# Performance work log

Hardware: AMD Instinct MI355X
Metric: run time of the kernel (lower is better)

## Reference

```python
import jax, jax.numpy as jnp
import numpy as np

N, E = 4096, 131072
IN_DIM, HID, OUT_DIM = 128, 64, 128
H1 = 4                       # gat1 heads
D_MODEL = HID * H1           # 256
NHEAD = 4
D_FF = 2048


def setup_inputs() -> dict:
    key = jax.random.key(0)
    ks = jax.random.split(key, 16)
    def w(k, shape, scale=0.05):
        return jax.random.normal(k, shape, dtype=jnp.float32) * scale
    return {
        "x": jax.random.normal(ks[0], (N, IN_DIM), dtype=jnp.float32),
        "edge_index": jax.random.randint(ks[1], (2, E), 0, N, dtype=jnp.int32),
        "gat1_w": w(ks[2], (H1 * HID, IN_DIM)),
        "gat1_asrc": w(ks[3], (H1, HID)),
        "gat1_adst": w(ks[4], (H1, HID)),
        "gat1_b": jnp.zeros((H1 * HID,), jnp.float32),
        "in_proj_w": w(ks[5], (3 * D_MODEL, D_MODEL)),
        "in_proj_b": jnp.zeros((3 * D_MODEL,), jnp.float32),
        "out_proj_w": w(ks[6], (D_MODEL, D_MODEL)),
        "out_proj_b": jnp.zeros((D_MODEL,), jnp.float32),
        "lin1_w": w(ks[7], (D_FF, D_MODEL)),
        "lin1_b": jnp.zeros((D_FF,), jnp.float32),
        "lin2_w": w(ks[8], (D_MODEL, D_FF)),
        "lin2_b": jnp.zeros((D_MODEL,), jnp.float32),
        "ln1_g": jnp.ones((D_MODEL,), jnp.float32),
        "ln1_b": jnp.zeros((D_MODEL,), jnp.float32),
        "ln2_g": jnp.ones((D_MODEL,), jnp.float32),
        "ln2_b": jnp.zeros((D_MODEL,), jnp.float32),
        "gat2_w": w(ks[9], (OUT_DIM, D_MODEL)),
        "gat2_asrc": w(ks[10], (1, OUT_DIM)),
        "gat2_adst": w(ks[11], (1, OUT_DIM)),
        "gat2_b": jnp.zeros((OUT_DIM,), jnp.float32),
    }


def _add_self_loops(ei, n):
    loops = jnp.arange(n, dtype=ei.dtype)
    return jnp.concatenate([ei, jnp.stack([loops, loops])], axis=1)


def _segment_softmax(logits, seg, n):
    # numerically stable softmax over edges grouped by destination node
    m = jax.ops.segment_max(logits, seg, num_segments=n)
    m = jnp.where(jnp.isfinite(m), m, 0.0)
    e = jnp.exp(logits - m[seg])
    s = jax.ops.segment_sum(e, seg, num_segments=n)
    return e / (s[seg] + 1e-16)


def _gat(x, ei, W, asrc, adst, b, heads, out_ch):
    n = x.shape[0]
    h = (x @ W.T).reshape(n, heads, out_ch)          # [N,H,C]
    al_s = jnp.einsum('nhc,hc->nh', h, asrc)
    al_d = jnp.einsum('nhc,hc->nh', h, adst)
    src, dst = ei[0], ei[1]
    logits = jax.nn.leaky_relu(al_s[src] + al_d[dst], 0.2)   # [E,H]
    alpha = _segment_softmax(logits, dst, n)
    out = jax.ops.segment_sum(h[src] * alpha[:, :, None], dst, num_segments=n)
    return out.reshape(n, heads * out_ch) + b


def _ln(x, g, b):
    mu = x.mean(-1, keepdims=True)
    v = x.var(-1, keepdims=True)
    return (x - mu) / jnp.sqrt(v + 1e-5) * g + b


def _forward(x, edge_index, gat1_w, gat1_asrc, gat1_adst, gat1_b,
             in_proj_w, in_proj_b, out_proj_w, out_proj_b,
             lin1_w, lin1_b, lin2_w, lin2_b, ln1_g, ln1_b, ln2_g, ln2_b,
             gat2_w, gat2_asrc, gat2_adst, gat2_b):
    n = x.shape[0]
    ei = _add_self_loops(edge_index, n)
    h = jax.nn.elu(_gat(x, ei, gat1_w, gat1_asrc, gat1_adst, gat1_b, H1, HID))  # [N, 256]
    # TransformerEncoderLayer (post-norm, relu, no dropout in eval)
    hd = D_MODEL // NHEAD
    qkv = h @ in_proj_w.T + in_proj_b
    q, k, v = jnp.split(qkv, 3, axis=-1)
    q = q.reshape(n, NHEAD, hd)
    k = k.reshape(n, NHEAD, hd)
    v = v.reshape(n, NHEAD, hd)
    scores = jnp.einsum('qhd,khd->hqk', q, k) / jnp.sqrt(jnp.float32(hd))
    attn = jax.nn.softmax(scores, axis=-1)
    o = jnp.einsum('hqk,khd->qhd', attn, v).reshape(n, D_MODEL)
    o = o @ out_proj_w.T + out_proj_b
    h = _ln(h + o, ln1_g, ln1_b)
    ff = jax.nn.relu(h @ lin1_w.T + lin1_b) @ lin2_w.T + lin2_b
    h = _ln(h + ff, ln2_g, ln2_b)
    return _gat(h, ei, gat2_w, gat2_asrc, gat2_adst, gat2_b, 1, OUT_DIM)


def reference(x, edge_index, gat1_w, gat1_asrc, gat1_adst, gat1_b,
              in_proj_w, in_proj_b, out_proj_w, out_proj_b,
              lin1_w, lin1_b, lin2_w, lin2_b, ln1_g, ln1_b, ln2_g, ln2_b,
              gat2_w, gat2_asrc, gat2_adst, gat2_b):
    return _forward(x, edge_index, gat1_w, gat1_asrc, gat1_adst, gat1_b,
                    in_proj_w, in_proj_b, out_proj_w, out_proj_b,
                    lin1_w, lin1_b, lin2_w, lin2_b, ln1_g, ln1_b, ln2_g, ln2_b,
                    gat2_w, gat2_asrc, gat2_adst, gat2_b)
```

## Files before the change

### kernel.cpp

```cpp
#include <hip/hip_runtime.h>
#include <hip/hip_bf16.h>
#include <math.h>

#define NN 4096
#define NE 131072
#define EE (NE + NN)

typedef unsigned short u16;
typedef short s8v __attribute__((ext_vector_type(8)));
typedef float f4v __attribute__((ext_vector_type(4)));
typedef float f16v __attribute__((ext_vector_type(16)));

__device__ inline u16 f2b(float f) {
  __hip_bfloat16 h = __float2bfloat16(f);
  return __builtin_bit_cast(u16, h);
}
__device__ inline float b2f(u16 v) {
  unsigned int u = ((unsigned int)v) << 16;
  return __builtin_bit_cast(float, u);
}

__global__ void k_count(const int* __restrict__ ei, int* __restrict__ deg) {
  int e = blockIdx.x * 256 + threadIdx.x;
  if (e >= EE) return;
  int dst = (e < NE) ? ei[NE + e] : (e - NE);
  atomicAdd(&deg[dst], 1);
}

__global__ __launch_bounds__(1024) void k_scan(const int* __restrict__ deg, int* __restrict__ rowptr) {
  __shared__ int lds[1024];
  int t = threadIdx.x;
  int v0 = deg[t*4+0], v1 = deg[t*4+1], v2 = deg[t*4+2], v3 = deg[t*4+3];
  int s1 = v0+v1, s2 = s1+v2, s3 = s2+v3;
  lds[t] = s3;
  __syncthreads();
  for (int off = 1; off < 1024; off <<= 1) {
    int add = (t >= off) ? lds[t-off] : 0;
    __syncthreads();
    lds[t] += add;
    __syncthreads();
  }
  int base = lds[t] - s3;
  rowptr[t*4+1] = base + v0;
  rowptr[t*4+2] = base + s1;
  rowptr[t*4+3] = base + s2;
  rowptr[t*4+4] = base + s3;
  if (t == 0) rowptr[0] = 0;
}

__global__ void k_scatter(const int* __restrict__ ei, const int* __restrict__ rowptr,
                          int* __restrict__ cursor, int* __restrict__ csr_src) {
  int e = blockIdx.x * 256 + threadIdx.x;
  if (e >= EE) return;
  int src, dst;
  if (e < NE) { src = ei[e]; dst = ei[NE + e]; }
  else { src = e - NE; dst = src; }
  int pos = rowptr[dst] + atomicAdd(&cursor[dst], 1);
  csr_src[pos] = src;
}

__global__ __launch_bounds__(256) void k_f2b_all(
    const float* a0, u16* b0, int e0, const float* a1, u16* b1, int e1,
    const float* a2, u16* b2, int e2, const float* a3, u16* b3, int e3,
    const float* a4, u16* b4, int e4, const float* a5, u16* b5, int e5,
    const float* a6, u16* b6, int e6)
{
  int i = blockIdx.x * 256 + threadIdx.x;
  const float* s; u16* d; int base;
  if      (i < e0) { s=a0; d=b0; base=0;  }
  else if (i < e1) { s=a1; d=b1; base=e0; }
  else if (i < e2) { s=a2; d=b2; base=e1; }
  else if (i < e3) { s=a3; d=b3; base=e2; }
  else if (i < e4) { s=a4; d=b4; base=e3; }
  else if (i < e5) { s=a5; d=b5; base=e4; }
  else if (i < e6) { s=a6; d=b6; base=e5; }
  else return;
  int j = i - base;
  float4 v = ((const float4*)s)[j];
  u16 r[4] = {f2b(v.x), f2b(v.y), f2b(v.z), f2b(v.w)};
  *(uint2*)(d + (size_t)j*4) = *(uint2*)r;
}

template<int HEADS, int C>
__global__ __launch_bounds__(256) void k_alogits(
    const u16* __restrict__ featb, const float* __restrict__ asrc,
    const float* __restrict__ adst, float* __restrict__ als, float* __restrict__ ald)
{
  constexpr int F = HEADS * C;
  int n = blockIdx.x, t = threadIdx.x;
  __shared__ float red[F];
  float f = b2f(featb[(size_t)n*F + t]);
  int hh = t / C, cc = t % C;
  red[t] = f * asrc[t];
  __syncthreads();
  for (int off = C/2; off > 0; off >>= 1) {
    float add = (cc < off) ? red[t + off] : 0.f;
    __syncthreads();
    if (cc < off) red[t] += add;
    __syncthreads();
  }
  if (cc == 0) als[(size_t)n*HEADS + hh] = red[t];
  __syncthreads();
  red[t] = f * adst[t];
  __syncthreads();
  for (int off = C/2; off > 0; off >>= 1) {
    float add = (cc < off) ? red[t + off] : 0.f;
    __syncthreads();
    if (cc < off) red[t] += add;
    __syncthreads();
  }
  if (cc == 0) ald[(size_t)n*HEADS + hh] = red[t];
}

template<int HEADS, int C, bool DO_ELU, bool WB>
__global__ __launch_bounds__(256) void k_gat_agg(
    const u16* __restrict__ featb, const float* __restrict__ als,
    const float* __restrict__ ald, const float* __restrict__ bias,
    const int* __restrict__ rowptr, const int* __restrict__ csr_src,
    float* __restrict__ out, u16* __restrict__ outb)
{
  constexpr int F = HEADS * C;
  int n = blockIdx.x, t = threadIdx.x;
  __shared__ float m_sh[HEADS], s_sh[HEADS];
  int start = rowptr[n];
  int deg = rowptr[n+1] - start;
  int lane = t & 63, wv = t >> 6;
  for (int hh = wv; hh < HEADS; hh += F/64) {
    float adl = ald[(size_t)n*HEADS + hh];
    float mx = -INFINITY;
    for (int i = lane; i < deg; i += 64) {
      int s = csr_src[start + i];
      float lg = als[(size_t)s*HEADS + hh] + adl;
      lg = (lg > 0.f) ? lg : 0.2f * lg;
      mx = fmaxf(mx, lg);
    }
    #pragma unroll
    for (int off = 32; off; off >>= 1) mx = fmaxf(mx, __shfl_xor(mx, off));
    float sm = 0.f;
    for (int i = lane; i < deg; i += 64) {
      int s = csr_src[start + i];
      float lg = als[(size_t)s*HEADS + hh] + adl;
      lg = (lg > 0.f) ? lg : 0.2f * lg;
      sm += expf(lg - mx);
    }
    #pragma unroll
    for (int off = 32; off; off >>= 1) sm += __shfl_xor(sm, off);
    if (lane == 0) { m_sh[hh] = mx; s_sh[hh] = sm; }
  }
  __syncthreads();
  int hh = t / C;
  float adl = ald[(size_t)n*HEADS + hh];
  float mh = m_sh[hh];
  float acc0 = 0.f, acc1 = 0.f;
  int i = 0;
  for (; i + 1 < deg; i += 2) {
    int s0 = csr_src[start + i];
    int s1 = csr_src[start + i + 1];
    float lg0 = als[(size_t)s0*HEADS + hh] + adl;
    float lg1 = als[(size_t)s1*HEADS + hh] + adl;
    lg0 = (lg0 > 0.f) ? lg0 : 0.2f * lg0;
    lg1 = (lg1 > 0.f) ? lg1 : 0.2f * lg1;
    float p0 = expf(lg0 - mh);
    float p1 = expf(lg1 - mh);
    acc0 += p0 * b2f(featb[(size_t)s0*F + t]);
    acc1 += p1 * b2f(featb[(size_t)s1*F + t]);
  }
  if (i < deg) {
    int s0 = csr_src[start + i];
    float lg0 = als[(size_t)s0*HEADS + hh] + adl;
    lg0 = (lg0 > 0.f) ? lg0 : 0.2f * lg0;
    acc0 += expf(lg0 - mh) * b2f(featb[(size_t)s0*F + t]);
  }
  float o = (acc0 + acc1) / (s_sh[hh] + 1e-16f) + bias[t];
  if (DO_ELU) o = (o > 0.f) ? o : (expf(o) - 1.f);
  out[(size_t)n*F + t] = o;
  if (WB) outb[(size_t)n*F + t] = f2b(o);
}

template<int MODE>
__global__ __launch_bounds__(256) void k_gemm_mfma(
    const u16* __restrict__ A, const u16* __restrict__ B,
    const float* __restrict__ bias, float* __restrict__ Cf, u16* __restrict__ Cb,
    u16* __restrict__ Qb, u16* __restrict__ Kb, u16* __restrict__ Vt,
    int M, int N, int K)
{
  __shared__ u16 Al[64*64];
  __shared__ u16 Bl[64*64];
  char* Ab = (char*)Al;
  char* Bb = (char*)Bl;
  const int t = threadIdx.x;
  const int lane = t & 63;
  const int lr = lane & 15, lk = lane >> 4;
  const int wid = t >> 6;
  const int wm = wid & 1, wn = wid >> 1;
  const int m0 = blockIdx.y * 64, n0 = blockIdx.x * 64;

  f4v acc[2][2];
  #pragma unroll
  for (int mi = 0; mi < 2; ++mi)
    #pragma unroll
    for (int ni = 0; ni < 2; ++ni)
      acc[mi][ni] = f4v{0.f, 0.f, 0.f, 0.f};

  for (int k0 = 0; k0 < K; k0 += 64) {
    #pragma unroll
    for (int i = 0; i < 2; ++i) {
      int idx = t + i*256;
      int row = idx >> 3, ch = idx & 7;
      s8v av = *(const s8v*)(A + (size_t)(m0 + row)*K + k0 + ch*8);
      *(s8v*)(Ab + row*128 + ((ch*16) ^ ((row & 7) << 4))) = av;
      s8v bv = *(const s8v*)(B + (size_t)(n0 + row)*K + k0 + ch*8);
      *(s8v*)(Bb + row*128 + ((ch*16) ^ ((row & 7) << 4))) = bv;
    }
    __syncthreads();
    #pragma unroll
    for (int ks = 0; ks < 2; ++ks) {
      s8v af[2], bfr[2];
      #pragma unroll
      for (int mi = 0; mi < 2; ++mi) {
        int row = wm*32 + mi*16 + lr;
        int ch = ks*4 + lk;
        af[mi] = *(const s8v*)(Ab + row*128 + ((ch*16) ^ ((row & 7) << 4)));
      }
      #pragma unroll
      for (int ni = 0; ni < 2; ++ni) {
        int row = wn*32 + ni*16 + lr;
        int ch = ks*4 + lk;
        bfr[ni] = *(const s8v*)(Bb + row*128 + ((ch*16) ^ ((row & 7) << 4)));
      }
      #pragma unroll
      for (int mi = 0; mi < 2; ++mi)
        #pragma unroll
        for (int ni = 0; ni < 2; ++ni)
          acc[mi][ni] = __builtin_amdgcn_mfma_f32_16x16x32_bf16(af[mi], bfr[ni], acc[mi][ni], 0, 0, 0);
    }
    __syncthreads();
  }
  #pragma unroll
  for (int ni = 0; ni < 2; ++ni) {
    int col = n0 + wn*32 + ni*16 + lr;
    float bc = bias ? bias[col] : 0.f;
    #pragma unroll
    for (int mi = 0; mi < 2; ++mi) {
      int row0 = m0 + wm*32 + mi*16 + lk*4;
      float v[4];
      #pragma unroll
      for (int r = 0; r < 4; ++r) {
        v[r] = acc[mi][ni][r] + bc;
        if (MODE == 1) v[r] = fmaxf(v[r], 0.f);
      }
      if (MODE == 0) {
        #pragma unroll
        for (int r = 0; r < 4; ++r) Cf[(size_t)(row0 + r)*N + col] = v[r];
      } else if (MODE == 1 || MODE == 2) {
        #pragma unroll
        for (int r = 0; r < 4; ++r) Cb[(size_t)(row0 + r)*N + col] = f2b(v[r]);
      } else {
        if (col < 512) {
          int head = (col >> 6) & 3;
          int d = col & 63;
          u16* dst = ((col < 256) ? Qb : Kb) + (size_t)head*262144 + d;
          #pragma unroll
          for (int r = 0; r < 4; ++r) dst[(size_t)(row0 + r)*64] = f2b(v[r]);
        } else {
          int cc = col - 512;
          int head = cc >> 6;
          int d = cc & 63;
          int quad = row0 & 12;
          int qs = (quad == 4) ? 8 : ((quad == 8) ? 4 : quad);
          size_t nphys = (size_t)((row0 & ~15) | qs);
          u16 o4[4];
          #pragma unroll
          for (int r = 0; r < 4; ++r) o4[r] = f2b(v[r]);
          *(uint2*)(Vt + (size_t)head*262144 + (size_t)d*4096 + nphys) = *(uint2*)o4;
        }
      }
    }
  }
}

__global__ __launch_bounds__(256) void k_gemm_sk(
    const u16* __restrict__ A, const u16* __restrict__ B,
    float* __restrict__ Po, int M, int N, int K)
{
  __shared__ u16 Al[64*64];
  __shared__ u16 Bl[64*64];
  char* Ab = (char*)Al;
  char* Bb = (char*)Bl;
  const int t = threadIdx.x;
  const int lane = t & 63;
  const int lr = lane & 15, lk = lane >> 4;
  const int wid = t >> 6;
  const int wm = wid & 1, wn = wid >> 1;
  const int m0 = blockIdx.y * 64, n0 = blockIdx.x * 64;
  const int z = blockIdx.z;
  const int ksl = K >> 2;

  f4v acc[2][2];
  #pragma unroll
  for (int mi = 0; mi < 2; ++mi)
    #pragma unroll
    for (int ni = 0; ni < 2; ++ni)
      acc[mi][ni] = f4v{0.f, 0.f, 0.f, 0.f};

  for (int k0 = z*ksl; k0 < (z+1)*ksl; k0 += 64) {
    #pragma unroll
    for (int i = 0; i < 2; ++i) {
      int idx = t + i*256;
      int row = idx >> 3, ch = idx & 7;
      s8v av = *(const s8v*)(A + (size_t)(m0 + row)*K + k0 + ch*8);
      *(s8v*)(Ab + row*128 + ((ch*16) ^ ((row & 7) << 4))) = av;
      s8v bv = *(const s8v*)(B + (size_t)(n0 + row)*K + k0 + ch*8);
      *(s8v*)(Bb + row*128 + ((ch*16) ^ ((row & 7) << 4))) = bv;
    }
    __syncthreads();
    #pragma unroll
    for (int ks = 0; ks < 2; ++ks) {
      s8v af[2], bfr[2];
      #pragma unroll
      for (int mi = 0; mi < 2; ++mi) {
        int row = wm*32 + mi*16 + lr;
        int ch = ks*4 + lk;
        af[mi] = *(const s8v*)(Ab + row*128 + ((ch*16) ^ ((row & 7) << 4)));
      }
      #pragma unroll
      for (int ni = 0; ni < 2; ++ni) {
        int row = wn*32 + ni*16 + lr;
        int ch = ks*4 + lk;
        bfr[ni] = *(const s8v*)(Bb + row*128 + ((ch*16) ^ ((row & 7) << 4)));
      }
      #pragma unroll
      for (int mi = 0; mi < 2; ++mi)
        #pragma unroll
        for (int ni = 0; ni < 2; ++ni)
          acc[mi][ni] = __builtin_amdgcn_mfma_f32_16x16x32_bf16(af[mi], bfr[ni], acc[mi][ni], 0, 0, 0);
    }
    __syncthreads();
  }
  float* Pz = Po + (size_t)z * M * N;
  #pragma unroll
  for (int ni = 0; ni < 2; ++ni) {
    int col = n0 + wn*32 + ni*16 + lr;
    #pragma unroll
    for (int mi = 0; mi < 2; ++mi) {
      int row0 = m0 + wm*32 + mi*16 + lk*4;
      #pragma unroll
      for (int r = 0; r < 4; ++r)
        Pz[(size_t)(row0 + r)*N + col] = acc[mi][ni][r];
    }
  }
}

template<bool WB>
__global__ __launch_bounds__(256) void k_ln(
    const float* __restrict__ a, const float* __restrict__ res,
    const float* __restrict__ g, const float* __restrict__ bb,
    float* __restrict__ out, u16* __restrict__ outb)
{
  int n = blockIdx.x, t = threadIdx.x;
  __shared__ float part[4];
  float v = a[(size_t)n*256 + t] + res[(size_t)n*256 + t];
  float s = v;
  #pragma unroll
  for (int off = 32; off; off >>= 1) s += __shfl_xor(s, off);
  if ((t & 63) == 0) part[t >> 6] = s;
  __syncthreads();
  float mean = (part[0] + part[1] + part[2] + part[3]) * (1.f/256.f);
  __syncthreads();
  float d = v - mean;
  float s2 = d * d;
  #pragma unroll
  for (int off = 32; off; off >>= 1) s2 += __shfl_xor(s2, off);
  if ((t & 63) == 0) part[t >> 6] = s2;
  __syncthreads();
  float var = (part[0] + part[1] + part[2] + part[3]) * (1.f/256.f);
  float rstd = rsqrtf(var + 1e-5f);
  float o = d * rstd * g[t] + bb[t];
  out[(size_t)n*256 + t] = o;
  if (WB) outb[(size_t)n*256 + t] = f2b(o);
}

template<bool WB>
__global__ __launch_bounds__(256) void k_ln_sk(
    const float* __restrict__ Po, const float* __restrict__ bias,
    const float* __restrict__ res, const float* __restrict__ g,
    const float* __restrict__ bb, float* __restrict__ out, u16* __restrict__ outb)
{
  int n = blockIdx.x, t = threadIdx.x;
  __shared__ float part[4];
  const size_t MN = (size_t)NN * 256;
  size_t idx = (size_t)n*256 + t;
  float v = Po[idx] + Po[MN + idx] + Po[2*MN + idx] + Po[3*MN + idx]
          + bias[t] + res[idx];
  float s = v;
  #pragma unroll
  for (int off = 32; off; off >>= 1) s += __shfl_xor(s, off);
  if ((t & 63) == 0) part[t >> 6] = s;
  __syncthreads();
  float mean = (part[0] + part[1] + part[2] + part[3]) * (1.f/256.f);
  __syncthreads();
  float d = v - mean;
  float s2 = d * d;
  #pragma unroll
  for (int off = 32; off; off >>= 1) s2 += __shfl_xor(s2, off);
  if ((t & 63) == 0) part[t >> 6] = s2;
  __syncthreads();
  float var = (part[0] + part[1] + part[2] + part[3]) * (1.f/256.f);
  float rstd = rsqrtf(var + 1e-5f);
  float o = d * rstd * g[t] + bb[t];
  out[idx] = o;
  if (WB) outb[idx] = f2b(o);
}

__global__ __launch_bounds__(512) void k_attn2(
    const u16* __restrict__ Qb, const u16* __restrict__ Kb,
    const u16* __restrict__ Vt, u16* __restrict__ attno_b)
{
  const int strip = blockIdx.x;
  const int head  = blockIdx.y;
  const int q0 = strip * 32;
  const int t = threadIdx.x;
  const int s = t >> 6;
  const int l = t & 63;
  const int lq = l & 31;
  const int lh = l >> 5;

  __shared__ float lds_O[4][32][68];
  __shared__ float lds_m[4][32];
  __shared__ float lds_l[4][32];

  const u16* Qh = Qb + (size_t)head * (4096*64);
  const u16* Kh = Kb + (size_t)head * (4096*64);
  const u16* Vh = Vt + (size_t)head * (64*4096);

  s8v qf[4];
#pragma unroll
  for (int dc = 0; dc < 4; ++dc)
    qf[dc] = *(const s8v*)(Qh + (size_t)(q0 + lq)*64 + dc*16 + lh*8);

  f16v accO[2];
#pragma unroll
  for (int dm = 0; dm < 2; ++dm)
#pragma unroll
    for (int i = 0; i < 16; ++i) accO[dm][i] = 0.f;

  float mrow = -INFINITY, lrow = 0.f;
  const float CE = 0.18033688011112042f;

  const int kt0 = s * 512;
  for (int kt = kt0; kt < kt0 + 512; kt += 64) {
    f16v st[2];
#pragma unroll
    for (int c = 0; c < 2; ++c)
#pragma unroll
      for (int i = 0; i < 16; ++i) st[c][i] = 0.f;
    __builtin_amdgcn_s_setprio(1);
#pragma unroll
    for (int dc = 0; dc < 4; ++dc) {
      s8v kf0 = *(const s8v*)(Kh + (size_t)(kt + lq)*64 + dc*16 + lh*8);
      s8v kf1 = *(const s8v*)(Kh + (size_t)(kt + 32 + lq)*64 + dc*16 + lh*8);
      st[0] = __builtin_amdgcn_mfma_f32_32x32x16_bf16(kf0, qf[dc], st[0], 0, 0, 0);
      st[1] = __builtin_amdgcn_mfma_f32_32x32x16_bf16(kf1, qf[dc], st[1], 0, 0, 0);
    }
    __builtin_amdgcn_s_setprio(0);
    float tm[16];
#pragma unroll
    for (int i = 0; i < 8; ++i) tm[i]   = fmaxf(st[0][2*i], st[0][2*i+1]);
#pragma unroll
    for (int i = 0; i < 8; ++i) tm[8+i] = fmaxf(st[1][2*i], st[1][2*i+1]);
#pragma unroll
    for (int w = 8; w >= 1; w >>= 1)
#pragma unroll
      for (int i = 0; i < 8; ++i) if (i < w) tm[i] = fmaxf(tm[i], tm[i+w]);
    float mx = fmaxf(tm[0], __shfl_xor(tm[0], 32));
    float mn;
    if (__all(mx - mrow <= 66.0f)) {
      mn = mrow;
    } else {
      mn = fmaxf(mrow, mx);
      float sc = exp2f((mrow - mn) * CE);
      mrow = mn;
      lrow *= sc;
#pragma unroll
      for (int dm = 0; dm < 2; ++dm)
#pragma unroll
        for (int i = 0; i < 16; ++i) accO[dm][i] *= sc;
    }
    float ts[16];
#pragma unroll
    for (int c = 0; c < 2; ++c)
#pragma unroll
      for (int i = 0; i < 16; ++i)
        st[c][i] = exp2f((st[c][i] - mn) * CE);
#pragma unroll
    for (int i = 0; i < 8; ++i) ts[i]   = st[0][2*i] + st[0][2*i+1];
#pragma unroll
    for (int i = 0; i < 8; ++i) ts[8+i] = st[1][2*i] + st[1][2*i+1];
#pragma unroll
    for (int w = 8; w >= 1; w >>= 1)
#pragma unroll
      for (int i = 0; i < 8; ++i) if (i < w) ts[i] += ts[i+w];
    float ps = ts[0] + __shfl_xor(ts[0], 32);
    lrow += ps;

#pragma unroll
    for (int c = 0; c < 2; ++c) {
#pragma unroll
      for (int kc = 0; kc < 2; ++kc) {
        union { s8v v; unsigned int w[4]; } pb;
#pragma unroll
        for (int wd = 0; wd < 4; ++wd) {
          u16 lo16 = f2b(st[c][kc*8 + wd*2]);
          u16 hi16 = f2b(st[c][kc*8 + wd*2 + 1]);
          pb.w[wd] = (unsigned int)lo16 | ((unsigned int)hi16 << 16);
        }
        __builtin_amdgcn_s_setprio(1);
#pragma unroll
        for (int dm = 0; dm < 2; ++dm) {
          s8v vf = *(const s8v*)(Vh + (size_t)(dm*32 + lq)*4096 + kt + c*32 + kc*16 + lh*8);
          accO[dm] = __builtin_amdgcn_mfma_f32_32x32x16_bf16(vf, pb.v, accO[dm], 0, 0, 0);
        }
        __builtin_amdgcn_s_setprio(0);
      }
    }
  }

#pragma unroll
  for (int lev = 0; lev < 3; ++lev) {
    const int step = 1 << lev;
    __syncthreads();
    if ((s & (2*step - 1)) == step) {
      int slot = (s - step) >> (lev + 1);
      if (l < 32) { lds_m[slot][lq] = mrow; lds_l[slot][lq] = lrow; }
#pragma unroll
      for (int dm = 0; dm < 2; ++dm)
#pragma unroll
        for (int g = 0; g < 4; ++g) {
          f4v v;
#pragma unroll
          for (int rr = 0; rr < 4; ++rr) v[rr] = accO[dm][g*4 + rr];
          *(f4v*)&lds_O[slot][lq][dm*32 + lh*4 + g*8] = v;
        }
    }
    __syncthreads();
    if ((s & (2*step - 1)) == 0) {
      int slot = s >> (lev + 1);
      float mp = lds_m[slot][lq], lp = lds_l[slot][lq];
      float M = fmaxf(mrow, mp);
      float w0 = exp2f((mrow - M) * CE);
      float w1 = exp2f((mp - M) * CE);
      lrow = lrow * w0 + lp * w1;
      mrow = M;
#pragma unroll
      for (int dm = 0; dm < 2; ++dm)
#pragma unroll
        for (int g = 0; g < 4; ++g) {
          f4v vp = *(const f4v*)&lds_O[slot][lq][dm*32 + lh*4 + g*8];
#pragma unroll
          for (int rr = 0; rr < 4; ++rr)
            accO[dm][g*4 + rr] = accO[dm][g*4 + rr] * w0 + vp[rr] * w1;
        }
    }
  }

  if (s == 0) {
    float inv = 1.f / lrow;
#pragma unroll
    for (int dm = 0; dm < 2; ++dm)
#pragma unroll
      for (int g = 0; g < 4; ++g) {
        u16 o4[4];
#pragma unroll
        for (int rr = 0; rr < 4; ++rr) o4[rr] = f2b(accO[dm][g*4 + rr] * inv);
        *(uint2*)(attno_b + (size_t)(q0 + lq)*256 + head*64 + dm*32 + lh*4 + g*8) = *(uint2*)o4;
      }
  }
}

extern "C" void kernel_launch(void* const* d_in, const int* in_sizes, int n_in,
                              void* d_out, int out_size, void* d_ws, size_t ws_size,
                              hipStream_t stream)
{
  const float* x       = (const float*)d_in[0];
  const int*   ei      = (const int*)d_in[1];
  const float* gat1_w  = (const float*)d_in[2];
  const float* gat1_as = (const float*)d_in[3];
  const float* gat1_ad = (const float*)d_in[4];
  const float* gat1_b  = (const float*)d_in[5];
  const float* inp_w   = (const float*)d_in[6];
  const float* inp_b   = (const float*)d_in[7];
  const float* outp_w  = (const float*)d_in[8];
  const float* outp_b  = (const float*)d_in[9];
  const float* lin1_w  = (const float*)d_in[10];
  const float* lin1_b  = (const float*)d_in[11];
  const float* lin2_w  = (const float*)d_in[12];
  const float* lin2_b  = (const float*)d_in[13];
  const float* ln1_g   = (const float*)d_in[14];
  const float* ln1_bb  = (const float*)d_in[15];
  const float* ln2_g   = (const float*)d_in[16];
  const float* ln2_bb  = (const float*)d_in[17];
  const float* gat2_w  = (const float*)d_in[18];
  const float* gat2_as = (const float*)d_in[19];
  const float* gat2_ad = (const float*)d_in[20];
  const float* gat2_b  = (const float*)d_in[21];
  float* out = (float*)d_out;
  (void)in_sizes; (void)n_in; (void)out_size; (void)ws_size;

  char* ws = (char*)d_ws;
  size_t off = 0;
  auto nxt = [&](size_t bytes) { size_t r = off; off += (bytes + 255) & ~(size_t)255; return r; };
  int* deg      = (int*)(ws + nxt((size_t)NN*4));
  int* cursor   = (int*)(ws + nxt((size_t)NN*4));
  int* rowptr   = (int*)(ws + nxt((size_t)(NN+1)*4));
  int* csr_src  = (int*)(ws + nxt((size_t)EE*4));
  float* al1s   = (float*)(ws + nxt((size_t)NN*4*4));
  float* al1d   = (float*)(ws + nxt((size_t)NN*4*4));
  float* hgat1  = (float*)(ws + nxt((size_t)NN*256*4));
  float* tmp256 = (float*)(ws + nxt((size_t)NN*256*4));
  float* hln1   = (float*)(ws + nxt((size_t)NN*256*4));
  float* hln2   = (float*)(ws + nxt((size_t)NN*256*4));
  float* Po     = (float*)(ws + nxt((size_t)4*NN*256*4));
  float* al2s   = (float*)(ws + nxt((size_t)NN*4));
  float* al2d   = (float*)(ws + nxt((size_t)NN*4));
  u16* x_b      = (u16*)(ws + nxt((size_t)NN*128*2));
  u16* feat1_b  = (u16*)(ws + nxt((size_t)NN*256*2));
  u16* feat2_b  = (u16*)(ws + nxt((size_t)NN*128*2));
  u16* hgat1_b  = (u16*)(ws + nxt((size_t)NN*256*2));
  u16* attno_b  = (u16*)(ws + nxt((size_t)NN*256*2));
  u16* hln1_b   = (u16*)(ws + nxt((size_t)NN*256*2));
  u16* hln2_b   = (u16*)(ws + nxt((size_t)NN*256*2));
  u16* ff1_b    = (u16*)(ws + nxt((size_t)NN*2048*2));
  u16* Qb       = (u16*)(ws + nxt((size_t)4*4096*64*2));
  u16* Kb       = (u16*)(ws + nxt((size_t)4*4096*64*2));
  u16* Vt       = (u16*)(ws + nxt((size_t)4*4096*64*2));
  u16* inp_w_b  = (u16*)(ws + nxt((size_t)768*256*2));
  u16* outp_w_b = (u16*)(ws + nxt((size_t)256*256*2));
  u16* lin1_w_b = (u16*)(ws + nxt((size_t)2048*256*2));
  u16* lin2_w_b = (u16*)(ws + nxt((size_t)256*2048*2));
  u16* gat1_w_b = (u16*)(ws + nxt((size_t)256*128*2));
  u16* gat2_w_b = (u16*)(ws + nxt((size_t)128*256*2));

  hipMemsetAsync(deg, 0, (size_t)NN*4, stream);
  hipMemsetAsync(cursor, 0, (size_t)NN*4, stream);
  k_count<<<(EE+255)/256, 256, 0, stream>>>(ei, deg);
  k_scan<<<1, 1024, 0, stream>>>(deg, rowptr);
  k_scatter<<<(EE+255)/256, 256, 0, stream>>>(ei, rowptr, cursor, csr_src);

  k_f2b_all<<<1856, 256, 0, stream>>>(
      inp_w,  inp_w_b,  49152,
      outp_w, outp_w_b, 65536,
      lin1_w, lin1_w_b, 196608,
      lin2_w, lin2_w_b, 327680,
      gat1_w, gat1_w_b, 335872,
      gat2_w, gat2_w_b, 344064,
      x,      x_b,      475136);

  k_gemm_mfma<2><<<dim3(4, 64), 256, 0, stream>>>(x_b, gat1_w_b, nullptr, nullptr, feat1_b, nullptr, nullptr, nullptr, NN, 256, 128);
  k_alogits<4,64><<<NN, 256, 0, stream>>>(feat1_b, gat1_as, gat1_ad, al1s, al1d);
  k_gat_agg<4,64,true,true><<<NN, 256, 0, stream>>>(feat1_b, al1s, al1d, gat1_b, rowptr, csr_src, hgat1, hgat1_b);

  k_gemm_mfma<3><<<dim3(12, 64), 256, 0, stream>>>(hgat1_b, inp_w_b, inp_b, nullptr, nullptr, Qb, Kb, Vt, NN, 768, 256);
  k_attn2<<<dim3(128, 4), 512, 0, stream>>>(Qb, Kb, Vt, attno_b);
  k_gemm_mfma<0><<<dim3(4, 64), 256, 0, stream>>>(attno_b, outp_w_b, outp_b, tmp256, nullptr, nullptr, nullptr, nullptr, NN, 256, 256);
  k_ln<true><<<NN, 256, 0, stream>>>(tmp256, hgat1, ln1_g, ln1_bb, hln1, hln1_b);
  k_gemm_mfma<1><<<dim3(32, 64), 256, 0, stream>>>(hln1_b, lin1_w_b, lin1_b, nullptr, ff1_b, nullptr, nullptr, nullptr, NN, 2048, 256);
  k_gemm_sk<<<dim3(4, 64, 4), 256, 0, stream>>>(ff1_b, lin2_w_b, Po, NN, 256, 2048);
  k_ln_sk<true><<<NN, 256, 0, stream>>>(Po, lin2_b, hln1, ln2_g, ln2_bb, hln2, hln2_b);

  k_gemm_mfma<2><<<dim3(2, 64), 256, 0, stream>>>(hln2_b, gat2_w_b, nullptr, nullptr, feat2_b, nullptr, nullptr, nullptr, NN, 128, 256);
  k_alogits<1,128><<<NN, 128, 0, stream>>>(feat2_b, gat2_as, gat2_ad, al2s, al2d);
  k_gat_agg<1,128,false,false><<<NN, 128, 0, stream>>>(feat2_b, al2s, al2d, gat2_b, rowptr, csr_src, out, nullptr);
}
```

Baseline: 307.6 us.

## Use wave shuffles in alogits, bigger GEMM tiles for FFN, prefetch K in attention

The attention-logit kernel now reduces with wave-level shuffles instead of shared-memory tree reductions with many barriers. The FFN GEMMs move to a new kernel with 128x64 tiles, where each wave covers 32 rows by 64 columns, to raise operand reuse and halve the block count. The flash-attention loop is unrolled by two and double-buffers K fragments in registers, and it loads V fragments ahead of the softmax to hide global latency. The online-max rescale condition is tightened to exact max tracking, which may add rescale work, and the larger tiles lower the number of blocks per GEMM.

```diff
diff --git a/kernel.cpp b/kernel.cpp
--- a/kernel.cpp
+++ b/kernel.cpp
@@ -88,28 +88,29 @@
 {
   constexpr int F = HEADS * C;
   int n = blockIdx.x, t = threadIdx.x;
-  __shared__ float red[F];
   float f = b2f(featb[(size_t)n*F + t]);
-  int hh = t / C, cc = t % C;
-  red[t] = f * asrc[t];
-  __syncthreads();
-  for (int off = C/2; off > 0; off >>= 1) {
-    float add = (cc < off) ? red[t + off] : 0.f;
-    __syncthreads();
-    if (cc < off) red[t] += add;
-    __syncthreads();
-  }
-  if (cc == 0) als[(size_t)n*HEADS + hh] = red[t];
-  __syncthreads();
-  red[t] = f * adst[t];
-  __syncthreads();
-  for (int off = C/2; off > 0; off >>= 1) {
-    float add = (cc < off) ? red[t + off] : 0.f;
-    __syncthreads();
-    if (cc < off) red[t] += add;
-    __syncthreads();
-  }
-  if (cc == 0) ald[(size_t)n*HEADS + hh] = red[t];
+  float ps = f * asrc[t];
+  float pd = f * adst[t];
+  #pragma unroll
+  for (int off = 32; off; off >>= 1) {
+    ps += __shfl_xor(ps, off);
+    pd += __shfl_xor(pd, off);
+  }
+  if constexpr (C == 64) {
+    if ((t & 63) == 0) {
+      int hh = t >> 6;
+      als[(size_t)n*HEADS + hh] = ps;
+      ald[(size_t)n*HEADS + hh] = pd;
+    }
+  } else {
+    __shared__ float sh[2][2];
+    if ((t & 63) == 0) { sh[t>>6][0] = ps; sh[t>>6][1] = pd; }
+    __syncthreads();
+    if (t == 0) {
+      als[n] = sh[0][0] + sh[1][0];
+      ald[n] = sh[0][1] + sh[1][1];
+    }
+  }
 }
 
 template<int HEADS, int C, bool DO_ELU, bool WB>
@@ -245,14 +246,11 @@
       int row0 = m0 + wm*32 + mi*16 + lk*4;
       float v[4];
       #pragma unroll
-      for (int r = 0; r < 4; ++r) {
-        v[r] = acc[mi][ni][r] + bc;
-        if (MODE == 1) v[r] = fmaxf(v[r], 0.f);
-      }
+      for (int r = 0; r < 4; ++r) v[r] = acc[mi][ni][r] + bc;
       if (MODE == 0) {
         #pragma unroll
         for (int r = 0; r < 4; ++r) Cf[(size_t)(row0 + r)*N + col] = v[r];
-      } else if (MODE == 1 || MODE == 2) {
+      } else if (MODE == 2) {
         #pragma unroll
         for (int r = 0; r < 4; ++r) Cb[(size_t)(row0 + r)*N + col] = f2b(v[r]);
       } else {
@@ -279,74 +277,87 @@
   }
 }
 
-__global__ __launch_bounds__(256) void k_gemm_sk(
+template<int MODE>
+__global__ __launch_bounds__(256) void k_gemm2(
     const u16* __restrict__ A, const u16* __restrict__ B,
-    float* __restrict__ Po, int M, int N, int K)
-{
-  __shared__ u16 Al[64*64];
+    const float* __restrict__ bias, float* __restrict__ Cf, u16* __restrict__ Cb,
+    int M, int N, int K, int ksl)
+{
+  __shared__ u16 Al[128*64];
   __shared__ u16 Bl[64*64];
   char* Ab = (char*)Al;
   char* Bb = (char*)Bl;
   const int t = threadIdx.x;
   const int lane = t & 63;
   const int lr = lane & 15, lk = lane >> 4;
-  const int wid = t >> 6;
-  const int wm = wid & 1, wn = wid >> 1;
-  const int m0 = blockIdx.y * 64, n0 = blockIdx.x * 64;
+  const int wv = t >> 6;
+  const int m0 = blockIdx.y * 128, n0 = blockIdx.x * 64;
   const int z = blockIdx.z;
-  const int ksl = K >> 2;
-
-  f4v acc[2][2];
+  const int kbeg = z * ksl, kend = kbeg + ksl;
+
+  f4v acc[2][4];
   #pragma unroll
   for (int mi = 0; mi < 2; ++mi)
     #pragma unroll
-    for (int ni = 0; ni < 2; ++ni)
+    for (int ni = 0; ni < 4; ++ni)
       acc[mi][ni] = f4v{0.f, 0.f, 0.f, 0.f};
 
-  for (int k0 = z*ksl; k0 < (z+1)*ksl; k0 += 64) {
-    #pragma unroll
-    for (int i = 0; i < 2; ++i) {
+  for (int k0 = kbeg; k0 < kend; k0 += 64) {
+    #pragma unroll
+    for (int i = 0; i < 4; ++i) {
       int idx = t + i*256;
       int row = idx >> 3, ch = idx & 7;
       s8v av = *(const s8v*)(A + (size_t)(m0 + row)*K + k0 + ch*8);
       *(s8v*)(Ab + row*128 + ((ch*16) ^ ((row & 7) << 4))) = av;
+    }
+    #pragma unroll
+    for (int i = 0; i < 2; ++i) {
+      int idx = t + i*256;
+      int row = idx >> 3, ch = idx & 7;
       s8v bv = *(const s8v*)(B + (size_t)(n0 + row)*K + k0 + ch*8);
       *(s8v*)(Bb + row*128 + ((ch*16) ^ ((row & 7) << 4))) = bv;
     }
     __syncthreads();
     #pragma unroll
     for (int ks = 0; ks < 2; ++ks) {
-      s8v af[2], bfr[2];
+      s8v af[2], bfr[4];
       #pragma unroll
       for (int mi = 0; mi < 2; ++mi) {
-        int row = wm*32 + mi*16 + lr;
+        int row = wv*32 + mi*16 + lr;
         int ch = ks*4 + lk;
         af[mi] = *(const s8v*)(Ab + row*128 + ((ch*16) ^ ((row & 7) << 4)));
       }
       #pragma unroll
-      for (int ni = 0; ni < 2; ++ni) {
-        int row = wn*32 + ni*16 + lr;
+      for (int ni = 0; ni < 4; ++ni) {
+        int row = ni*16 + lr;
         int ch = ks*4 + lk;
         bfr[ni] = *(const s8v*)(Bb + row*128 + ((ch*16) ^ ((row & 7) << 4)));
       }
       #pragma unroll
       for (int mi = 0; mi < 2; ++mi)
         #pragma unroll
-        for (int ni = 0; ni < 2; ++ni)
+        for (int ni = 0; ni < 4; ++ni)
           acc[mi][ni] = __builtin_amdgcn_mfma_f32_16x16x32_bf16(af[mi], bfr[ni], acc[mi][ni], 0, 0, 0);
     }
     __syncthreads();
   }
-  float* Pz = Po + (size_t)z * M * N;
-  #pragma unroll
-  for (int ni = 0; ni < 2; ++ni) {
-    int col = n0 + wn*32 + ni*16 + lr;
+  #pragma unroll
+  for (int ni = 0; ni < 4; ++ni) {
+    int col = n0 + ni*16 + lr;
+    float bc = (MODE == 4) ? 0.f : bias[col];
     #pragma unroll
     for (int mi = 0; mi < 2; ++mi) {
-      int row0 = m0 + wm*32 + mi*16 + lk*4;
-      #pragma unroll
-      for (int r = 0; r < 4; ++r)
-        Pz[(size_t)(row0 + r)*N + col] = acc[mi][ni][r];
+      int row0 = m0 + wv*32 + mi*16 + lk*4;
+      #pragma unroll
+      for (int r = 0; r < 4; ++r) {
+        float v = acc[mi][ni][r] + bc;
+        if (MODE == 1) {
+          v = fmaxf(v, 0.f);
+          Cb[(size_t)(row0 + r)*N + col] = f2b(v);
+        } else {
+          (Cf + (size_t)z*M*N)[(size_t)(row0 + r)*N + col] = v;
+        }
+      }
     }
   }
 }
@@ -411,6 +422,86 @@
   out[idx] = o;
   if (WB) outb[idx] = f2b(o);
 }
+
+#define LOADK(KB, ktn) do { \
+  _Pragma("unroll") \
+  for (int dc = 0; dc < 4; ++dc) { \
+    KB[dc*2+0] = *(const s8v*)(Kh + (size_t)((ktn) + lq)*64 + dc*16 + lh*8); \
+    KB[dc*2+1] = *(const s8v*)(Kh + (size_t)((ktn) + 32 + lq)*64 + dc*16 + lh*8); \
+  } \
+} while (0)
+
+#define TILE(ktc, KB) do { \
+  f16v st0, st1; \
+  _Pragma("unroll") \
+  for (int i = 0; i < 16; ++i) { st0[i] = 0.f; st1[i] = 0.f; } \
+  _Pragma("unroll") \
+  for (int dc = 0; dc < 4; ++dc) { \
+    st0 = __builtin_amdgcn_mfma_f32_32x32x16_bf16(KB[dc*2+0], qf[dc], st0, 0, 0, 0); \
+    st1 = __builtin_amdgcn_mfma_f32_32x32x16_bf16(KB[dc*2+1], qf[dc], st1, 0, 0, 0); \
+  } \
+  s8v vb[8]; \
+  _Pragma("unroll") \
+  for (int c = 0; c < 2; ++c) \
+    _Pragma("unroll") \
+    for (int kc = 0; kc < 2; ++kc) \
+      _Pragma("unroll") \
+      for (int dm = 0; dm < 2; ++dm) \
+        vb[(c*2+kc)*2+dm] = *(const s8v*)(Vh + (size_t)(dm*32 + lq)*4096 + (ktc) + c*32 + kc*16 + lh*8); \
+  float tm[16]; \
+  _Pragma("unroll") \
+  for (int i = 0; i < 8; ++i) tm[i]   = fmaxf(st0[2*i], st0[2*i+1]); \
+  _Pragma("unroll") \
+  for (int i = 0; i < 8; ++i) tm[8+i] = fmaxf(st1[2*i], st1[2*i+1]); \
+  _Pragma("unroll") \
+  for (int w = 8; w >= 1; w >>= 1) \
+    _Pragma("unroll") \
+    for (int i = 0; i < 8; ++i) if (i < w) tm[i] = fmaxf(tm[i], tm[i+w]); \
+  float mx = fmaxf(tm[0], __shfl_xor(tm[0], 32)); \
+  float mn; \
+  if (__all(mx <= mrow)) { \
+    mn = mrow; \
+  } else { \
+    mn = fmaxf(mrow, mx); \
+    float sc = exp2f((mrow - mn) * CE); \
+    mrow = mn; \
+    lrow *= sc; \
+    _Pragma("unroll") \
+    for (int dm = 0; dm < 2; ++dm) \
+      _Pragma("unroll") \
+      for (int i = 0; i < 16; ++i) accO[dm][i] *= sc; \
+  } \
+  float ts[16]; \
+  _Pragma("unroll") \
+  for (int i = 0; i < 16; ++i) st0[i] = exp2f((st0[i] - mn) * CE); \
+  _Pragma("unroll") \
+  for (int i = 0; i < 16; ++i) st1[i] = exp2f((st1[i] - mn) * CE); \
+  _Pragma("unroll") \
+  for (int i = 0; i < 8; ++i) ts[i]   = st0[2*i] + st0[2*i+1]; \
+  _Pragma("unroll") \
+  for (int i = 0; i < 8; ++i) ts[8+i] = st1[2*i] + st1[2*i+1]; \
+  _Pragma("unroll") \
+  for (int w = 8; w >= 1; w >>= 1) \
+    _Pragma("unroll") \
+    for (int i = 0; i < 8; ++i) if (i < w) ts[i] += ts[i+w]; \
+  lrow += ts[0] + __shfl_xor(ts[0], 32); \
+  _Pragma("unroll") \
+  for (int c = 0; c < 2; ++c) { \
+    _Pragma("unroll") \
+    for (int kc = 0; kc < 2; ++kc) { \
+      union { s8v v; unsigned int w[4]; } pb; \
+      _Pragma("unroll") \
+      for (int wd = 0; wd < 4; ++wd) { \
+        float e0 = (c == 0) ? st0[kc*8 + wd*2]     : st1[kc*8 + wd*2]; \
+        float e1 = (c == 0) ? st0[kc*8 + wd*2 + 1] : st1[kc*8 + wd*2 + 1]; \
+        pb.w[wd] = (unsigned int)f2b(e0) | ((unsigned int)f2b(e1) << 16); \
+      } \
+      _Pragma("unroll") \
+      for (int dm = 0; dm < 2; ++dm) \
+        accO[dm] = __builtin_amdgcn_mfma_f32_32x32x16_bf16(vb[(c*2+kc)*2+dm], pb.v, accO[dm], 0, 0, 0); \
+    } \
+  } \
+} while (0)
 
 __global__ __launch_bounds__(512) void k_attn2(
     const u16* __restrict__ Qb, const u16* __restrict__ Kb,
@@ -448,81 +539,15 @@
   const float CE = 0.18033688011112042f;
 
   const int kt0 = s * 512;
-  for (int kt = kt0; kt < kt0 + 512; kt += 64) {
-    f16v st[2];
-#pragma unroll
-    for (int c = 0; c < 2; ++c)
-#pragma unroll
-      for (int i = 0; i < 16; ++i) st[c][i] = 0.f;
-    __builtin_amdgcn_s_setprio(1);
-#pragma unroll
-    for (int dc = 0; dc < 4; ++dc) {
-      s8v kf0 = *(const s8v*)(Kh + (size_t)(kt + lq)*64 + dc*16 + lh*8);
-      s8v kf1 = *(const s8v*)(Kh + (size_t)(kt + 32 + lq)*64 + dc*16 + lh*8);
-      st[0] = __builtin_amdgcn_mfma_f32_32x32x16_bf16(kf0, qf[dc], st[0], 0, 0, 0);
-      st[1] = __builtin_amdgcn_mfma_f32_32x32x16_bf16(kf1, qf[dc], st[1], 0, 0, 0);
-    }
-    __builtin_amdgcn_s_setprio(0);
-    float tm[16];
-#pragma unroll
-    for (int i = 0; i < 8; ++i) tm[i]   = fmaxf(st[0][2*i], st[0][2*i+1]);
-#pragma unroll
-    for (int i = 0; i < 8; ++i) tm[8+i] = fmaxf(st[1][2*i], st[1][2*i+1]);
-#pragma unroll
-    for (int w = 8; w >= 1; w >>= 1)
-#pragma unroll
-      for (int i = 0; i < 8; ++i) if (i < w) tm[i] = fmaxf(tm[i], tm[i+w]);
-    float mx = fmaxf(tm[0], __shfl_xor(tm[0], 32));
-    float mn;
-    if (__all(mx - mrow <= 66.0f)) {
-      mn = mrow;
-    } else {
-      mn = fmaxf(mrow, mx);
-      float sc = exp2f((mrow - mn) * CE);
-      mrow = mn;
-      lrow *= sc;
-#pragma unroll
-      for (int dm = 0; dm < 2; ++dm)
-#pragma unroll
-        for (int i = 0; i < 16; ++i) accO[dm][i] *= sc;
-    }
-    float ts[16];
-#pragma unroll
-    for (int c = 0; c < 2; ++c)
-#pragma unroll
-      for (int i = 0; i < 16; ++i)
-        st[c][i] = exp2f((st[c][i] - mn) * CE);
-#pragma unroll
-    for (int i = 0; i < 8; ++i) ts[i]   = st[0][2*i] + st[0][2*i+1];
-#pragma unroll
-    for (int i = 0; i < 8; ++i) ts[8+i] = st[1][2*i] + st[1][2*i+1];
-#pragma unroll
-    for (int w = 8; w >= 1; w >>= 1)
-#pragma unroll
-      for (int i = 0; i < 8; ++i) if (i < w) ts[i] += ts[i+w];
-    float ps = ts[0] + __shfl_xor(ts[0], 32);
-    lrow += ps;
-
-#pragma unroll
-    for (int c = 0; c < 2; ++c) {
-#pragma unroll
-      for (int kc = 0; kc < 2; ++kc) {
-        union { s8v v; unsigned int w[4]; } pb;
-#pragma unroll
-        for (int wd = 0; wd < 4; ++wd) {
-          u16 lo16 = f2b(st[c][kc*8 + wd*2]);
-          u16 hi16 = f2b(st[c][kc*8 + wd*2 + 1]);
-          pb.w[wd] = (unsigned int)lo16 | ((unsigned int)hi16 << 16);
-        }
-        __builtin_amdgcn_s_setprio(1);
-#pragma unroll
-        for (int dm = 0; dm < 2; ++dm) {
-          s8v vf = *(const s8v*)(Vh + (size_t)(dm*32 + lq)*4096 + kt + c*32 + kc*16 + lh*8);
-          accO[dm] = __builtin_amdgcn_mfma_f32_32x32x16_bf16(vf, pb.v, accO[dm], 0, 0, 0);
-        }
-        __builtin_amdgcn_s_setprio(0);
-      }
-    }
+  s8v kbA[8], kbB[8];
+  LOADK(kbA, kt0);
+  for (int kt = kt0; kt < kt0 + 512; kt += 128) {
+    LOADK(kbB, kt + 64);
+    TILE(kt, kbA);
+    int ktn = kt + 128;
+    if (ktn >= kt0 + 512) ktn = kt0;
+    LOADK(kbA, ktn);
+    TILE(kt + 64, kbB);
   }
 
 #pragma unroll
@@ -663,8 +688,8 @@
   k_attn2<<<dim3(128, 4), 512, 0, stream>>>(Qb, Kb, Vt, attno_b);
   k_gemm_mfma<0><<<dim3(4, 64), 256, 0, stream>>>(attno_b, outp_w_b, outp_b, tmp256, nullptr, nullptr, nullptr, nullptr, NN, 256, 256);
   k_ln<true><<<NN, 256, 0, stream>>>(tmp256, hgat1, ln1_g, ln1_bb, hln1, hln1_b);
-  k_gemm_mfma<1><<<dim3(32, 64), 256, 0, stream>>>(hln1_b, lin1_w_b, lin1_b, nullptr, ff1_b, nullptr, nullptr, nullptr, NN, 2048, 256);
-  k_gemm_sk<<<dim3(4, 64, 4), 256, 0, stream>>>(ff1_b, lin2_w_b, Po, NN, 256, 2048);
+  k_gemm2<1><<<dim3(32, 32), 256, 0, stream>>>(hln1_b, lin1_w_b, lin1_b, nullptr, ff1_b, NN, 2048, 256, 256);
+  k_gemm2<4><<<dim3(4, 32, 4), 256, 0, stream>>>(ff1_b, lin2_w_b, nullptr, Po, nullptr, NN, 256, 2048, 512);
   k_ln_sk<true><<<NN, 256, 0, stream>>>(Po, lin2_b, hln1, ln2_g, ln2_bb, hln2, hln2_b);
 
   k_gemm_mfma<2><<<dim3(2, 64), 256, 0, stream>>>(hln2_b, gat2_w_b, nullptr, nullptr, feat2_b, nullptr, nullptr, nullptr, NN, 128, 256);
```

New measurement: 306.2 us. Within noise of the previous version (-0.4%).
